# Optimization experiments

Hardware: AMD Instinct MI355X
Metric: run time of the kernel (lower is better)

The kernel has to match this reference:

```python
import jax, jax.numpy as jnp
import numpy as np

B, H, W, D = 2, 64, 64, 512
D_HEAD = 64
N_HEADS = D // D_HEAD
KERNEL = 7


def make_neighbourhood_mask(kernel: int, canvas_h: int, canvas_w: int) -> jnp.ndarray:
    """Boolean [HW, HW] mask: query (i,j) attends to a clamped kernel x kernel window."""
    h_ramp = jnp.arange(canvas_h)
    w_ramp = jnp.arange(canvas_w)
    h_pos, w_pos = jnp.meshgrid(h_ramp, w_ramp, indexing='ij')
    start_h = jnp.clip(h_pos - kernel // 2, 0, canvas_h - kernel)[..., None, None]
    end_h = start_h + kernel
    start_w = jnp.clip(w_pos - kernel // 2, 0, canvas_w - kernel)[..., None, None]
    end_w = start_w + kernel
    h_range = h_ramp.reshape(1, 1, canvas_h, 1)
    w_range = w_ramp.reshape(1, 1, 1, canvas_w)
    mask = (h_range >= start_h) & (h_range < end_h) & (w_range >= start_w) & (w_range < end_w)
    return mask.reshape(canvas_h * canvas_w, canvas_h * canvas_w)


def setup_inputs() -> dict:
    key = jax.random.key(0)
    k1, k2, k3 = jax.random.split(key, 3)
    x = jax.random.normal(k1, (B, H, W, D), dtype=jnp.float32)
    w_qkv = jax.random.normal(k2, (3 * D, D), dtype=jnp.float32) * (D ** -0.5)
    w_out = jax.random.normal(k3, (D, D), dtype=jnp.float32) * (D ** -0.5)
    return {"x": x, "w_qkv": w_qkv, "w_out": w_out}


def reference(x, w_qkv, w_out):
    b, h, w, d = x.shape
    s = h * w
    # qkv projection (Linear, no bias): [b,h,w,3d]
    qkv = jnp.einsum('bhwd,ed->bhwe', x, w_qkv)
    # split per torch rearrange 'n h w (t nh e) -> t n nh (h w) e'
    qkv = qkv.reshape(b, s, 3, N_HEADS, D_HEAD).transpose(2, 0, 3, 1, 4)  # [3,b,nh,s,e]
    q, k, v = qkv[0], qkv[1], qkv[2]
    mask = make_neighbourhood_mask(KERNEL, h, w)  # [s, s] bool
    scale = D_HEAD ** -0.5
    scores = jnp.einsum('bnse,bnte->bnst', q, k) * scale  # [b,nh,s,s]
    neg_inf = jnp.finfo(scores.dtype).min
    scores = jnp.where(mask[None, None, :, :], scores, neg_inf)
    attn = jax.nn.softmax(scores, axis=-1)
    out = jnp.einsum('bnst,bnte->bnse', attn, v)  # [b,nh,s,e]
    out = out.transpose(0, 2, 1, 3).reshape(b, h, w, d)  # [b,h,w,d]
    return jnp.einsum('bhwd,ed->bhwe', out, w_out)
```

## Files before the change

kernel.cpp:

```cpp
#include <hip/hip_runtime.h>
#include <hip/hip_bf16.h>


typedef __bf16 bf16x8 __attribute__((ext_vector_type(8)));
typedef __bf16 bf16x4 __attribute__((ext_vector_type(4)));
typedef __bf16 bf16x2 __attribute__((ext_vector_type(2)));
typedef float  f32x4  __attribute__((ext_vector_type(4)));
typedef int    i32x4  __attribute__((ext_vector_type(4)));

__global__ __launch_bounds__(256) void cvt_all(
    const float* __restrict__ x, const float* __restrict__ wq,
    const float* __restrict__ wo, __bf16* __restrict__ xb,
    __bf16* __restrict__ wqb, __bf16* __restrict__ wob) {
  int i = blockIdx.x * 256 + threadIdx.x;
  const float* src;
  __bf16* dst;
  int j = i;
  if (j < 524288) {
    src = x; dst = xb;
  } else if (j < 524288 + 98304) {
    j -= 524288; src = wq; dst = wqb;
  } else {
    j -= 524288 + 98304; src = wo; dst = wob;
  }
  f32x4 v0 = ((const f32x4*)src)[j * 2];
  f32x4 v1 = ((const f32x4*)src)[j * 2 + 1];
  bf16x8 o;
  o[0] = (__bf16)v0[0]; o[1] = (__bf16)v0[1];
  o[2] = (__bf16)v0[2]; o[3] = (__bf16)v0[3];
  o[4] = (__bf16)v1[0]; o[5] = (__bf16)v1[1];
  o[6] = (__bf16)v1[2]; o[7] = (__bf16)v1[3];
  ((bf16x8*)dst)[j] = o;
}

__device__ __forceinline__ void gload_lds16(const __bf16* g, __bf16* l) {
  __builtin_amdgcn_global_load_lds(
      (const __attribute__((address_space(1))) void*)g,
      (__attribute__((address_space(3))) void*)l, 16, 0, 0);
}

template <bool QKV, int BN>
__global__ __launch_bounds__(256, 3) void gemm_lds(
    const __bf16* __restrict__ A, const __bf16* __restrict__ W,
    __bf16* __restrict__ qo, __bf16* __restrict__ ko, __bf16* __restrict__ vo,
    float* __restrict__ co, int etiles) {
  constexpr int K = 512;
  constexpr int NT = BN / 32;
  constexpr int WHALF = BN * 32;
  __shared__ alignas(16) __bf16 shm[2 * 128 * 32 + 2 * WHALF];
  __bf16* Al = shm;
  __bf16* Wl = shm + 2 * 128 * 32;
  __bf16* ct = shm;
  const int tid = threadIdx.x;
  const int wv = tid >> 6, lane = tid & 63;
  const int n16 = lane & 15, quad = lane >> 4;
  const int nper = (int)gridDim.x >> 3;
  const int wg = (blockIdx.x & 7) * nper + (blockIdx.x >> 3);
  const int bi = wg / etiles, be = wg % etiles;
  const int i0 = bi << 7, e0 = be * BN;
  const int wm = (wv & 1) << 6, we = (wv >> 1) * (BN / 2);

  const int srow = (wv << 4) + (lane >> 2);
  const int scol = (lane & 3) << 3;
  const __bf16* gA = A + (size_t)(i0 + srow) * K + scol;
  const __bf16* gW = W + (size_t)(e0 + srow) * K + scol;
  const int soff = (wv << 9) + (lane << 3);

  f32x4 acc[4][NT];
#pragma unroll
  for (int a = 0; a < 4; ++a)
#pragma unroll
    for (int b = 0; b < NT; ++b) acc[a][b] = (f32x4){0.f, 0.f, 0.f, 0.f};

  for (int k0 = 0; k0 < K; k0 += 64) {
    if (k0) __syncthreads();
#pragma unroll
    for (int h = 0; h < 2; ++h) {
      gload_lds16(gA + k0 + h * 32, &Al[h * 4096 + soff]);
      gload_lds16(gA + (size_t)64 * K + k0 + h * 32,
                  &Al[h * 4096 + 64 * 32 + soff]);
      gload_lds16(gW + k0 + h * 32, &Wl[h * WHALF + soff]);
      if (BN == 128)
        gload_lds16(gW + (size_t)64 * K + k0 + h * 32,
                    &Wl[h * WHALF + 64 * 32 + soff]);
    }
    __syncthreads();

#pragma unroll
    for (int h = 0; h < 2; ++h) {
      bf16x8 af[4], wf[NT];
#pragma unroll
      for (int t = 0; t < 4; ++t)
        af[t] = *(const bf16x8*)&Al[h * 4096 + (wm + t * 16 + n16) * 32 +
                                    quad * 8];
#pragma unroll
      for (int t = 0; t < NT; ++t)
        wf[t] = *(const bf16x8*)&Wl[h * WHALF + (we + t * 16 + n16) * 32 +
                                    quad * 8];
#pragma unroll
      for (int mt = 0; mt < 4; ++mt)
#pragma unroll
        for (int nt = 0; nt < NT; ++nt)
          acc[mt][nt] = __builtin_amdgcn_mfma_f32_16x16x32_bf16(
              af[mt], wf[nt], acc[mt][nt], 0, 0, 0);
    }
  }

  if (QKV) {
    __syncthreads();
    const int tsel = e0 >> 9;
    if (tsel == 2) {
#pragma unroll
      for (int mt = 0; mt < 4; ++mt)
#pragma unroll
        for (int nt = 0; nt < NT; ++nt) {
          f32x4 f = acc[mt][nt];
          int el = we + nt * 16 + n16;
          int il = wm + mt * 16 + quad * 4;
          bf16x4 h4 = {(__bf16)f[0], (__bf16)f[1], (__bf16)f[2], (__bf16)f[3]};
          *(bf16x4*)&ct[el * 128 + (il ^ ((el & 7) << 3))] = h4;
        }
    } else {
      const float qs = (tsel == 0) ? 0.125f : 1.0f;
#pragma unroll
      for (int mt = 0; mt < 4; ++mt)
#pragma unroll
        for (int nt = 0; nt < NT; ++nt) {
          f32x4 f = acc[mt][nt];
          int el = we + nt * 16 + n16;
#pragma unroll
          for (int rg = 0; rg < 4; ++rg) {
            int il = wm + mt * 16 + quad * 4 + rg;
            ct[il * 128 + (el ^ ((il & 7) << 3))] = (__bf16)(f[rg] * qs);
          }
        }
    }
    __syncthreads();
    const int b = i0 >> 12;
    const int s0 = i0 & 4095;
#pragma unroll
    for (int u = 0; u < 8; ++u) {
      int cid = u * 256 + tid;
      int row = cid >> 4, c8 = (cid & 15) << 3;
      bf16x8 d = *(const bf16x8*)&ct[row * 128 + (c8 ^ ((row & 7) << 3))];
      if (tsel == 2) {
        int e = e0 + row;
        int head = (e >> 6) & 7, dh = e & 63;
        *(bf16x8*)&vo[((size_t)(b * 8 + head) * 64 + dh) * 4096 + s0 + c8] = d;
      } else {
        int e = e0 + c8;
        int head = (e >> 6) & 7, dh = e & 63;
        size_t off = ((size_t)(b * 8 + head) * 4096 + (s0 + row)) * 64 + dh;
        *(bf16x8*)&((tsel == 0) ? qo : ko)[off] = d;
      }
    }
  } else {
#pragma unroll
    for (int mt = 0; mt < 4; ++mt)
#pragma unroll
      for (int nt = 0; nt < NT; ++nt) {
        f32x4 f = acc[mt][nt];
        int e = e0 + we + nt * 16 + n16;
#pragma unroll
        for (int rg = 0; rg < 4; ++rg) {
          int i = i0 + wm + mt * 16 + quad * 4 + rg;
          co[(size_t)i * 512 + e] = f[rg];
        }
      }
  }
}

__global__ __launch_bounds__(256, 4) void attn_mfma(
    const __bf16* __restrict__ q, const __bf16* __restrict__ k,
    const __bf16* __restrict__ vt, __bf16* __restrict__ out) {
  __shared__ alignas(16) __bf16 r1[14848];
  const int tid = threadIdx.x;
  const int wv = tid >> 6;
  const int lane = tid & 63;
  const int n16 = lane & 15, quad = lane >> 4;
  const int wg = ((blockIdx.x & 7) << 7) + (blockIdx.x >> 3);
  const int bh = wg >> 6;
  const int tile = wg & 63;
  const int qh0 = (tile >> 3) << 3, qw0 = (tile & 7) << 3;
  int wh0 = qh0 - 3; wh0 = wh0 < 0 ? 0 : (wh0 > 50 ? 50 : wh0);
  int wc0 = qw0 - 3; wc0 = wc0 < 0 ? 0 : (wc0 > 48 ? 48 : wc0);
  wc0 &= ~1;
  const size_t base = (size_t)bh * 4096 * 64;

  const int qi = wv * 16 + n16;
  const int sq = (qh0 + (qi >> 3)) * 64 + qw0 + (qi & 7);
  const __bf16* qp = q + base + (size_t)sq * 64 + quad * 8;
  bf16x8 bq0 = *(const bf16x8*)qp;
  bf16x8 bq1 = *(const bf16x8*)(qp + 32);

  const __bf16* kbase = k + base;
#pragma unroll
  for (int i = 0; i < 7; ++i) {
    int ch = i * 256 + tid;
    int kr = ch >> 7, wi = ch & 127;
    int kc = wi >> 3, dh8 = wi & 7;
    gload_lds16(kbase + (size_t)((wh0 + kr) * 64 + wc0 + kc) * 64 +
                    ((dh8 ^ (kc & 7)) * 8),
                &r1[ch * 8]);
  }
  __syncthreads();

  f32x4 S[14];
  const int sw1 = ((quad ^ (n16 & 7)) * 8);
  const int sw2 = (((4 + quad) ^ (n16 & 7)) * 8);
#pragma unroll
  for (int nt = 0; nt < 14; ++nt) {
    int key = nt * 16 + n16;
    bf16x8 kf0 = *(const bf16x8*)&r1[key * 64 + sw1];
    bf16x8 kf1 = *(const bf16x8*)&r1[key * 64 + sw2];
    f32x4 s = {0.f, 0.f, 0.f, 0.f};
    s = __builtin_amdgcn_mfma_f32_16x16x32_bf16(kf0, bq0, s, 0, 0, 0);
    s = __builtin_amdgcn_mfma_f32_16x16x32_bf16(kf1, bq1, s, 0, 0, 0);
    S[nt] = s;
  }

  const int qh = qh0 + (qi >> 3), qw = qw0 + (qi & 7);
  int sh = qh - 3; sh = sh < 0 ? 0 : (sh > 57 ? 57 : sh);
  int sw = qw - 3; sw = sw < 0 ? 0 : (sw > 57 ? 57 : sw);
  const int lo = sh - wh0;
  bool wok[4];
#pragma unroll
  for (int reg = 0; reg < 4; ++reg) {
    int kw = wc0 + quad * 4 + reg;
    wok[reg] = (kw >= sw) && (kw < sw + 7);
  }
  float mx[4] = {-1e30f, -1e30f, -1e30f, -1e30f};
#pragma unroll
  for (int nt = 0; nt < 14; ++nt) {
    bool rok = (unsigned)(nt - lo) < 7u;
#pragma unroll
    for (int reg = 0; reg < 4; ++reg) {
      float val = (rok && wok[reg]) ? S[nt][reg] : -1e30f;
      S[nt][reg] = val;
      mx[reg] = mx[reg] > val ? mx[reg] : val;
    }
  }
  float m = fmaxf(fmaxf(mx[0], mx[1]), fmaxf(mx[2], mx[3]));
  m = fmaxf(m, __shfl_xor(m, 16));
  m = fmaxf(m, __shfl_xor(m, 32));

  int plo[14], phi[14];
  float sm[4] = {0.f, 0.f, 0.f, 0.f};
#pragma unroll
  for (int nt = 0; nt < 14; ++nt) {
    float p0 = __expf(S[nt][0] - m);
    float p1 = __expf(S[nt][1] - m);
    float p2 = __expf(S[nt][2] - m);
    float p3 = __expf(S[nt][3] - m);
    sm[0] += p0; sm[1] += p1; sm[2] += p2; sm[3] += p3;
    bf16x2 a = {(__bf16)p0, (__bf16)p1};
    bf16x2 b = {(__bf16)p2, (__bf16)p3};
    plo[nt] = __builtin_bit_cast(int, a);
    phi[nt] = __builtin_bit_cast(int, b);
  }
  float ssum = (sm[0] + sm[1]) + (sm[2] + sm[3]);
  ssum += __shfl_xor(ssum, 16);
  ssum += __shfl_xor(ssum, 32);
  const float inv = 1.f / ssum;

  __syncthreads();
  const __bf16* vtb = vt + base;
#pragma unroll
  for (int i = 0; i < 7; ++i) {
    int c = i * 256 + tid;
    int dh = c / 28, rem = c % 28;
    int kr = rem >> 1, half = rem & 1;
    bf16x8 d = *(const bf16x8*)(vtb + (size_t)dh * 4096 +
                                (wh0 + kr) * 64 + wc0 + half * 8);
    *(bf16x8*)&r1[dh * 232 + kr * 16 + half * 8] = d;
  }
  __syncthreads();

  f32x4 O[4] = {{0.f, 0.f, 0.f, 0.f},
                {0.f, 0.f, 0.f, 0.f},
                {0.f, 0.f, 0.f, 0.f},
                {0.f, 0.f, 0.f, 0.f}};
  const int s0 = ((quad & 1) << 5) + n16;
  const int s1 = s0 + 16;
  const bool hiq = quad >= 2;
#pragma unroll
  for (int kt = 0; kt < 7; ++kt) {
    const int nA = 2 * kt, nB = 2 * kt + 1;
    int a0 = __shfl(plo[nA], s0), a1 = __shfl(phi[nA], s0);
    int a2 = __shfl(plo[nA], s1), a3 = __shfl(phi[nA], s1);
    int b0 = __shfl(plo[nB], s0), b1 = __shfl(phi[nB], s0);
    int b2 = __shfl(plo[nB], s1), b3 = __shfl(phi[nB], s1);
    i32x4 pu = {hiq ? b0 : a0, hiq ? b1 : a1, hiq ? b2 : a2, hiq ? b3 : a3};
    bf16x8 pa = __builtin_bit_cast(bf16x8, pu);
    const int key0 = kt * 32 + quad * 8;
#pragma unroll
    for (int ntv = 0; ntv < 4; ++ntv) {
      bf16x8 vb = *(const bf16x8*)&r1[(ntv * 16 + n16) * 232 + key0];
      O[ntv] = __builtin_amdgcn_mfma_f32_16x16x32_bf16(pa, vb, O[ntv], 0, 0, 0);
    }
  }

  float invr[4];
#pragma unroll
  for (int reg = 0; reg < 4; ++reg) invr[reg] = __shfl(inv, quad * 4 + reg);

  const int b = bh >> 3, head = bh & 7;
#pragma unroll
  for (int ntv = 0; ntv < 4; ++ntv)
#pragma unroll
    for (int reg = 0; reg < 4; ++reg) {
      int qe = wv * 16 + quad * 4 + reg;
      int s_q = (qh0 + (qe >> 3)) * 64 + qw0 + (qe & 7);
      int dh = ntv * 16 + n16;
      out[((size_t)(b * 4096 + s_q)) * 512 + head * 64 + dh] =
          (__bf16)(O[ntv][reg] * invr[reg]);
    }
}

extern "C" void kernel_launch(void* const* d_in, const int* in_sizes, int n_in,
                              void* d_out, int out_size, void* d_ws,
                              size_t ws_size, hipStream_t stream) {
  const float* x = (const float*)d_in[0];
  const float* w_qkv = (const float*)d_in[1];
  const float* w_out = (const float*)d_in[2];
  float* out = (float*)d_out;

  const size_t qelems = (size_t)2 * 8 * 4096 * 64;
  __bf16* q = (__bf16*)d_ws;
  __bf16* k = q + qelems;
  __bf16* vt = k + qelems;
  __bf16* xb = vt + qelems;
  __bf16* wqb = xb + qelems;
  __bf16* wob = wqb + 1536 * 512;
  __bf16* ao = xb;

  cvt_all<<<dim3(2560), dim3(256), 0, stream>>>(x, w_qkv, w_out, xb, wqb, wob);

  gemm_lds<true, 128><<<dim3(768), dim3(256), 0, stream>>>(
      xb, wqb, q, k, vt, nullptr, 12);
  attn_mfma<<<dim3(1024), dim3(256), 0, stream>>>(q, k, vt, ao);
  gemm_lds<false, 64><<<dim3(512), dim3(256), 0, stream>>>(
      ao, wob, nullptr, nullptr, nullptr, out, 8);
}
```

Measured before the change: 113.9 us.

## Prefetch next K-tile during MFMA in GEMM and use nontemporal stores

Restructures the projection GEMM loop so that A/W fragments are read from LDS into registers first, then the next K-tile's global-to-LDS loads are issued before the MFMAs run. This overlaps global memory latency with compute. Output stores in the GEMM and attention kernels are also switched to nontemporal stores. These may bypass cache for data that the next kernel reads immediately, which could hurt reuse. The change also raises register pressure by holding two halves of fragments.

```diff
diff --git a/kernel.cpp b/kernel.cpp
--- a/kernel.cpp
+++ b/kernel.cpp
@@ -37,6 +37,10 @@
   __builtin_amdgcn_global_load_lds(
       (const __attribute__((address_space(1))) void*)g,
       (__attribute__((address_space(3))) void*)l, 16, 0, 0);
+}
+
+__device__ __forceinline__ void nt_store16(const bf16x8& v, __bf16* p) {
+  __builtin_nontemporal_store(__builtin_bit_cast(i32x4, v), (i32x4*)p);
 }
 
 template <bool QKV, int BN>
@@ -72,38 +76,52 @@
 #pragma unroll
     for (int b = 0; b < NT; ++b) acc[a][b] = (f32x4){0.f, 0.f, 0.f, 0.f};
 
+#pragma unroll
+  for (int h = 0; h < 2; ++h) {
+    gload_lds16(gA + h * 32, &Al[h * 4096 + soff]);
+    gload_lds16(gA + (size_t)64 * K + h * 32, &Al[h * 4096 + 2048 + soff]);
+    gload_lds16(gW + h * 32, &Wl[h * WHALF + soff]);
+    if (BN == 128)
+      gload_lds16(gW + (size_t)64 * K + h * 32,
+                  &Wl[h * WHALF + 2048 + soff]);
+  }
+
   for (int k0 = 0; k0 < K; k0 += 64) {
-    if (k0) __syncthreads();
+    __syncthreads();
+    bf16x8 af[2][4], wf[2][NT];
 #pragma unroll
     for (int h = 0; h < 2; ++h) {
-      gload_lds16(gA + k0 + h * 32, &Al[h * 4096 + soff]);
-      gload_lds16(gA + (size_t)64 * K + k0 + h * 32,
-                  &Al[h * 4096 + 64 * 32 + soff]);
-      gload_lds16(gW + k0 + h * 32, &Wl[h * WHALF + soff]);
-      if (BN == 128)
-        gload_lds16(gW + (size_t)64 * K + k0 + h * 32,
-                    &Wl[h * WHALF + 64 * 32 + soff]);
+#pragma unroll
+      for (int t = 0; t < 4; ++t)
+        af[h][t] = *(const bf16x8*)&Al[h * 4096 + (wm + t * 16 + n16) * 32 +
+                                       quad * 8];
+#pragma unroll
+      for (int t = 0; t < NT; ++t)
+        wf[h][t] = *(const bf16x8*)&Wl[h * WHALF + (we + t * 16 + n16) * 32 +
+                                       quad * 8];
     }
     __syncthreads();
-
-#pragma unroll
-    for (int h = 0; h < 2; ++h) {
-      bf16x8 af[4], wf[NT];
-#pragma unroll
-      for (int t = 0; t < 4; ++t)
-        af[t] = *(const bf16x8*)&Al[h * 4096 + (wm + t * 16 + n16) * 32 +
-                                    quad * 8];
-#pragma unroll
-      for (int t = 0; t < NT; ++t)
-        wf[t] = *(const bf16x8*)&Wl[h * WHALF + (we + t * 16 + n16) * 32 +
-                                    quad * 8];
+    if (k0 + 64 < K) {
+      const int kn = k0 + 64;
+#pragma unroll
+      for (int h = 0; h < 2; ++h) {
+        gload_lds16(gA + kn + h * 32, &Al[h * 4096 + soff]);
+        gload_lds16(gA + (size_t)64 * K + kn + h * 32,
+                    &Al[h * 4096 + 2048 + soff]);
+        gload_lds16(gW + kn + h * 32, &Wl[h * WHALF + soff]);
+        if (BN == 128)
+          gload_lds16(gW + (size_t)64 * K + kn + h * 32,
+                      &Wl[h * WHALF + 2048 + soff]);
+      }
+    }
+#pragma unroll
+    for (int h = 0; h < 2; ++h)
 #pragma unroll
       for (int mt = 0; mt < 4; ++mt)
 #pragma unroll
         for (int nt = 0; nt < NT; ++nt)
           acc[mt][nt] = __builtin_amdgcn_mfma_f32_16x16x32_bf16(
-              af[mt], wf[nt], acc[mt][nt], 0, 0, 0);
-    }
+              af[h][mt], wf[h][nt], acc[mt][nt], 0, 0, 0);
   }
 
   if (QKV) {
@@ -146,12 +164,12 @@
       if (tsel == 2) {
         int e = e0 + row;
         int head = (e >> 6) & 7, dh = e & 63;
-        *(bf16x8*)&vo[((size_t)(b * 8 + head) * 64 + dh) * 4096 + s0 + c8] = d;
+        nt_store16(d, &vo[((size_t)(b * 8 + head) * 64 + dh) * 4096 + s0 + c8]);
       } else {
         int e = e0 + c8;
         int head = (e >> 6) & 7, dh = e & 63;
         size_t off = ((size_t)(b * 8 + head) * 4096 + (s0 + row)) * 64 + dh;
-        *(bf16x8*)&((tsel == 0) ? qo : ko)[off] = d;
+        nt_store16(d, &((tsel == 0) ? qo : ko)[off]);
       }
     }
   } else {
@@ -164,7 +182,7 @@
 #pragma unroll
         for (int rg = 0; rg < 4; ++rg) {
           int i = i0 + wm + mt * 16 + quad * 4 + rg;
-          co[(size_t)i * 512 + e] = f[rg];
+          __builtin_nontemporal_store(f[rg], &co[(size_t)i * 512 + e]);
         }
       }
   }
@@ -312,8 +330,9 @@
       int qe = wv * 16 + quad * 4 + reg;
       int s_q = (qh0 + (qe >> 3)) * 64 + qw0 + (qe & 7);
       int dh = ntv * 16 + n16;
-      out[((size_t)(b * 4096 + s_q)) * 512 + head * 64 + dh] =
-          (__bf16)(O[ntv][reg] * invr[reg]);
+      __builtin_nontemporal_store(
+          (__bf16)(O[ntv][reg] * invr[reg]),
+          &out[((size_t)(b * 4096 + s_q)) * 512 + head * 64 + dh]);
     }
 }
 
```

New measurement: 119.8 us. 1.05x slower.
